# Kernel tuning notes

Hardware: AMD Instinct MI355X
Metric: run time of the kernel (lower is better)

Reference implementation:

```python
import jax, jax.numpy as jnp
import numpy as np

B, IN_DIM, OUT_DIM = 16384, 1024, 512
N_CAPS, CAP_DIM = 8, 16


def squash(x, axis=-1):
    # scale = |x|^2 / (1 + |x|^2) ; out = scale * x / sqrt(|x|^2 + 1e-8)
    sq = jnp.sum(x * x, axis=axis, keepdims=True)
    return (sq / (1.0 + sq)) * x / jnp.sqrt(sq + 1e-8)


def setup_inputs() -> dict:
    key = jax.random.key(0)
    k1, k2, k3, k4 = jax.random.split(key, 4)
    x = jax.random.normal(k1, (B, IN_DIM), dtype=jnp.float32)
    # Linear(in_dim, n_caps*cap_dim) params (kaiming-ish scale)
    Wp = jax.random.normal(k2, (IN_DIM, N_CAPS * CAP_DIM), dtype=jnp.float32) / np.sqrt(IN_DIM)
    bp = jax.random.normal(k3, (N_CAPS * CAP_DIM,), dtype=jnp.float32) * 0.01
    # routing transform W: [n_caps, cap_dim, out_dim], init std 0.02 as in torch code
    W = jax.random.normal(k4, (N_CAPS, CAP_DIM, OUT_DIM), dtype=jnp.float32) * 0.02
    return {"x": x, "Wp": Wp, "bp": bp, "W": W, "n_routing": 3}


def reference(x, Wp, bp, W, n_routing):
    batch = x.shape[0]
    primary = x @ Wp + bp                                   # [B, n*d]
    primary = primary.reshape(batch, N_CAPS, CAP_DIM)       # [B, n, d]
    primary = squash(primary, axis=-1)
    u_hat = jnp.einsum('bnd,ndo->bno', primary, W)          # [B, n, o]
    b = jnp.zeros((batch, N_CAPS, 1), dtype=x.dtype)
    v = None
    for i in range(n_routing):
        c = jax.nn.softmax(b, axis=1)                       # [B, n, 1]
        s = jnp.sum(c * u_hat, axis=1)                      # [B, o]
        v = squash(s, axis=-1)                              # [B, o]
        if i < n_routing - 1:
            agreement = jnp.einsum('bno,bo->bn', u_hat, v)  # [B, n]
            b = b + agreement[..., None]
    return v
```

## Files before the change

kernel.cpp:

```cpp
#include <hip/hip_runtime.h>
#include <hip/hip_bf16.h>
#include <math.h>

typedef __attribute__((ext_vector_type(8))) short bf16x8;
typedef __attribute__((ext_vector_type(8))) unsigned short u16x8;
typedef __attribute__((ext_vector_type(4))) float f32x4;
typedef __attribute__((ext_vector_type(16))) float f32x16;

__device__ __forceinline__ unsigned short f2bf(float f) {
  unsigned u = __float_as_uint(f);
  return (unsigned short)((u + 0x7FFFu + ((u >> 16) & 1u)) >> 16);
}
__device__ __forceinline__ float bf2f(unsigned short h) {
  return __uint_as_float(((unsigned)h) << 16);
}
__device__ __forceinline__ void cvt8pk_a(const float* f, u16x8& h, u16x8& l) {
  unsigned* hp = (unsigned*)&h;
  unsigned* lp = (unsigned*)&l;
#pragma unroll
  for (int i = 0; i < 4; ++i) {
    __hip_bfloat162 hb = __float22bfloat162_rn(make_float2(f[2*i], f[2*i+1]));
    unsigned hv = *(unsigned*)&hb;
    hp[i] = hv;
    float r0 = f[2*i]     - __uint_as_float(hv << 16);
    float r1 = f[2*i + 1] - __uint_as_float(hv & 0xFFFF0000u);
    __hip_bfloat162 lb = __float22bfloat162_rn(make_float2(r0, r1));
    lp[i] = *(unsigned*)&lb;
  }
}
__device__ __forceinline__ void cvt8pk(const float4& a, const float4& b,
                                       u16x8& h, u16x8& l) {
  float f[8] = {a.x, a.y, a.z, a.w, b.x, b.y, b.z, b.w};
  cvt8pk_a(f, h, l);
}
__device__ __forceinline__ void cvt8b(const float4& a, const float4& b,
                                      bf16x8& h, bf16x8& l) {
  u16x8 hh, ll;
  cvt8pk(a, b, hh, ll);
  h = *(bf16x8*)&hh;
  l = *(bf16x8*)&ll;
}

#define GLD16(g, l) __builtin_amdgcn_global_load_lds( \
    (const __attribute__((address_space(1))) void*)(g), \
    (__attribute__((address_space(3))) void*)(l), 16, 0, 0)

#define MFMA32(a, b, c) __builtin_amdgcn_mfma_f32_32x32x16_bf16(a, b, c, 0, 0, 0)

__global__ __launch_bounds__(256) void caps_prep_all(
    const float* __restrict__ Wp, const float* __restrict__ W,
    unsigned short* __restrict__ th1, unsigned short* __restrict__ tl1,
    unsigned short* __restrict__ th2, unsigned short* __restrict__ tl2,
    unsigned short* __restrict__ th3, unsigned short* __restrict__ tl3)
{
  __shared__ float tile[64][128];
  const int t = threadIdx.x, b = blockIdx.x;
  if (b < 16) {
    const float* src = Wp + (size_t)b * 64 * 128;
#pragma unroll
    for (int i = 0; i < 8; ++i) {
      int j = t + i * 256;
      int kk = j >> 5, q = j & 31;
      *(float4*)&tile[kk][q * 4] = *(const float4*)(src + kk * 128 + q * 4);
    }
    __syncthreads();
    const int col = t >> 1, kg0 = (t & 1) * 4;
    unsigned short hi[32], lo[32];
#pragma unroll
    for (int kk = 0; kk < 32; ++kk) {
      float v = tile[kg0 * 8 + kk][col];
      unsigned short h = f2bf(v);
      hi[kk] = h;
      lo[kk] = f2bf(v - bf2f(h));
    }
#pragma unroll
    for (int i = 0; i < 4; ++i) {
      size_t off = (size_t)b * 8192 + (size_t)(kg0 + i) * 1024 + (size_t)col * 8;
      u16x8 vh, vl;
#pragma unroll
      for (int e = 0; e < 8; ++e) { vh[e] = hi[i * 8 + e]; vl[e] = lo[i * 8 + e]; }
      *(u16x8*)(th1 + off) = vh;
      *(u16x8*)(tl1 + off) = vl;
    }
  } else if (b < 32) {
    int tt = (b - 16) * 256 + t;
#pragma unroll
    for (int h = 0; h < 2; ++h) {
      int c = tt + h * 4096;
      int kt = c >> 12, rem = c & 4095;
      int kg = rem >> 9, col = rem & 511;
      int kbase = kt * 64 + kg * 8;
      u16x8 vh, vl;
#pragma unroll
      for (int e = 0; e < 8; ++e) {
        float v = W[(size_t)(kbase + e) * 512 + col];
        unsigned short hh = f2bf(v);
        vh[e] = hh;
        vl[e] = f2bf(v - bf2f(hh));
      }
      size_t off = ((size_t)(kt * 8 + kg) * 512 + col) * 8;
      *(u16x8*)(th2 + off) = vh;
      *(u16x8*)(tl2 + off) = vl;
    }
  } else {
    int bb = b - 32;
    int a = (bb >> 3) * 16 + (t >> 4);
    int c = (bb & 7) * 16 + (t & 15);
    const float* wa = W + (size_t)a * 512;
    const float* wb = W + (size_t)c * 512;
    float acc = 0.f;
#pragma unroll 4
    for (int o = 0; o < 512; o += 4) {
      float4 xx = *(const float4*)(wa + o);
      float4 yy = *(const float4*)(wb + o);
      acc += xx.x * yy.x + xx.y * yy.y + xx.z * yy.z + xx.w * yy.w;
    }
    unsigned short h = f2bf(acc);
    unsigned short l = f2bf(acc - bf2f(h));
    size_t off = ((size_t)(a >> 3) * 128 + c) * 8 + (a & 7);
    th3[off] = h;
    tl3[off] = l;
  }
}

#define K1BUF 20480

__global__ __launch_bounds__(256) void caps_primary(
    const float* __restrict__ x, const unsigned short* __restrict__ bth,
    const unsigned short* __restrict__ btl, const float* __restrict__ bp,
    float* __restrict__ p_out)
{
  __shared__ unsigned short lds[2 * K1BUF];
  const int tid  = threadIdx.x;
  const int lane = tid & 63;
  const int wn   = tid >> 6;
  const int lc   = lane & 31;
  const int hi   = lane >> 5;
  const int row0 = blockIdx.x * 32;

  const int rowA = tid & 31;
  const int kgA  = tid >> 5;
  const float* xrow = x + (size_t)(row0 + rowA) * 1024 + kgA * 8;

  f32x16 acc;
#pragma unroll
  for (int j = 0; j < 16; ++j) acc[j] = 0.f;

  float4 a0, a1;

#define A_LOAD(kt) do { const float* xp_ = xrow + (kt) * 64; \
    a0 = *(const float4*)(xp_); a1 = *(const float4*)(xp_ + 4); } while (0)

#define B_ISSUE(kt, bufi) do { \
    unsigned short* Bh_ = lds + (bufi) * K1BUF + 4096; \
    unsigned short* Bl_ = lds + (bufi) * K1BUF + 12288; \
    const unsigned short* gh_ = bth + ((size_t)(kt) * 1024 + tid) * 8; \
    const unsigned short* gl_ = btl + ((size_t)(kt) * 1024 + tid) * 8; \
    _Pragma("unroll") for (int c_ = 0; c_ < 4; ++c_) { \
      GLD16(gh_ + c_ * 2048, Bh_ + (c_ * 256 + tid) * 8); \
      GLD16(gl_ + c_ * 2048, Bl_ + (c_ * 256 + tid) * 8); \
    } } while (0)

#define A_WRITE(bufi) do { u16x8 h_, l_; cvt8pk(a0, a1, h_, l_); \
    unsigned short* A_ = lds + (bufi) * K1BUF; \
    *(u16x8*)(A_ + (kgA * 32 + rowA) * 8) = h_; \
    *(u16x8*)(A_ + 2048 + (kgA * 32 + rowA) * 8) = l_; } while (0)

#define COMPUTE(bufi) do { \
    const unsigned short* F = lds + (bufi) * K1BUF; \
    _Pragma("unroll") \
    for (int kk = 0; kk < 4; ++kk) { \
      const int ks = kk * 2 + hi; \
      bf16x8 ah  = *(const bf16x8*)(F + (ks * 32 + lc) * 8); \
      bf16x8 al  = *(const bf16x8*)(F + 2048 + (ks * 32 + lc) * 8); \
      bf16x8 bh  = *(const bf16x8*)(F + 4096  + (ks * 128 + wn * 32 + lc) * 8); \
      bf16x8 blo = *(const bf16x8*)(F + 12288 + (ks * 128 + wn * 32 + lc) * 8); \
      acc = MFMA32(ah, bh,  acc); \
      acc = MFMA32(ah, blo, acc); \
      acc = MFMA32(al, bh,  acc); \
    } } while (0)

  A_LOAD(0);
  B_ISSUE(0, 0);
  A_WRITE(0);
  __syncthreads();

#pragma unroll 2
  for (int kt = 0; kt < 16; ++kt) {
    const int cur = kt & 1;
    if (kt < 15) {
      A_LOAD(kt + 1);
      B_ISSUE(kt + 1, cur ^ 1);
    }
    COMPUTE(cur);
    if (kt < 15) A_WRITE(cur ^ 1);
    __syncthreads();
  }
#undef A_LOAD
#undef B_ISSUE
#undef A_WRITE
#undef COMPUTE

  const int col = wn * 32 + lc;
  const float bpv = bp[col];
#pragma unroll
  for (int r = 0; r < 16; ++r) {
    const int row = (r & 3) + 8 * (r >> 2) + 4 * hi;
    float val = acc[r] + bpv;
    float sq = val * val;
    sq += __shfl_xor(sq, 1); sq += __shfl_xor(sq, 2);
    sq += __shfl_xor(sq, 4); sq += __shfl_xor(sq, 8);
    float sc = (sq / (1.f + sq)) / sqrtf(sq + 1e-8f);
    p_out[(size_t)(row0 + row) * 128 + col] = val * sc;
  }
}

__global__ __launch_bounds__(512) void caps_route_g(
    const float* __restrict__ p_in, const unsigned short* __restrict__ mh,
    const unsigned short* __restrict__ ml, float* __restrict__ cs_out)
{
  __shared__ float pT[128 * 65];
  __shared__ unsigned short Msh[32768];
  __shared__ float t_lds[64 * 9];
  __shared__ float c_lds[64 * 9];
  const int tid  = threadIdx.x;
  const int lane = tid & 63;
  const int w    = tid >> 6;
  const int wm   = w >> 2;
  const int wn   = w & 3;
  const int lc   = lane & 31;
  const int hi   = lane >> 5;
  const int row0 = blockIdx.x * 64;

#pragma unroll
  for (int i = 0; i < 4; ++i) {
    int idx = tid + i * 512;
    *(u16x8*)&Msh[idx * 8] = *(const u16x8*)(mh + (size_t)idx * 8);
    *(u16x8*)&Msh[16384 + idx * 8] = *(const u16x8*)(ml + (size_t)idx * 8);
  }
#pragma unroll
  for (int i = 0; i < 4; ++i) {
    int j = tid + i * 512;
    int r = j >> 5, c4 = j & 31;
    f32x4 v = *(const f32x4*)(p_in + (size_t)(row0 + r) * 128 + c4 * 4);
    pT[(c4 * 4 + 0) * 65 + r] = v[0];
    pT[(c4 * 4 + 1) * 65 + r] = v[1];
    pT[(c4 * 4 + 2) * 65 + r] = v[2];
    pT[(c4 * 4 + 3) * 65 + r] = v[3];
  }
  if (w == 0) {
#pragma unroll
    for (int n = 0; n < 8; ++n) c_lds[lane * 9 + n] = 0.125f;
  }
  __syncthreads();

  const int arow = wm * 32 + lc;
  const int col  = wn * 32 + lc;
  const int cap  = wn * 2 + (lc >> 4);
  float bb[8] = {0.f, 0.f, 0.f, 0.f, 0.f, 0.f, 0.f, 0.f};

#pragma unroll 1
  for (int it = 0; it < 3; ++it) {
    f32x16 acc;
#pragma unroll
    for (int j = 0; j < 16; ++j) acc[j] = 0.f;

#pragma unroll
    for (int kk = 0; kk < 8; ++kk) {
      const float cv = c_lds[arow * 9 + kk];
      float q[8];
#pragma unroll
      for (int e = 0; e < 8; ++e)
        q[e] = pT[(kk * 16 + hi * 8 + e) * 65 + arow] * cv;
      u16x8 hq, lq;
      cvt8pk_a(q, hq, lq);
      const int fi = ((kk * 2 + hi) * 128 + col) * 8;
      bf16x8 mbh = *(const bf16x8*)&Msh[fi];
      bf16x8 mbl = *(const bf16x8*)&Msh[16384 + fi];
      acc = MFMA32(*(bf16x8*)&hq, mbh, acc);
      acc = MFMA32(*(bf16x8*)&hq, mbl, acc);
      acc = MFMA32(*(bf16x8*)&lq, mbh, acc);
    }

    float tp[16];
#pragma unroll
    for (int r = 0; r < 16; ++r) {
      const int row = wm * 32 + (r & 3) + 8 * (r >> 2) + 4 * hi;
      float prod = pT[col * 65 + row] * acc[r];
      prod += __shfl_xor(prod, 1);
      prod += __shfl_xor(prod, 2);
      prod += __shfl_xor(prod, 4);
      prod += __shfl_xor(prod, 8);
      tp[r] = prod;
    }
    __syncthreads();
    if ((lc & 15) == 0) {
#pragma unroll
      for (int r = 0; r < 16; ++r) {
        const int row = wm * 32 + (r & 3) + 8 * (r >> 2) + 4 * hi;
        t_lds[row * 9 + cap] = tp[r];
      }
    }
    __syncthreads();

    if (w == 0) {
      float c[8], t[8];
#pragma unroll
      for (int n = 0; n < 8; ++n) {
        c[n] = c_lds[lane * 9 + n];
        t[n] = t_lds[lane * 9 + n];
      }
      float ss = 0.f;
#pragma unroll
      for (int n = 0; n < 8; ++n) ss = fmaf(c[n], t[n], ss);
      float scale = (ss / (1.f + ss)) / sqrtf(ss + 1e-8f);
      if (it < 2) {
#pragma unroll
        for (int n = 0; n < 8; ++n) bb[n] += scale * t[n];
        float mx = bb[0];
#pragma unroll
        for (int n = 1; n < 8; ++n) mx = fmaxf(mx, bb[n]);
        float e[8], Z = 0.f;
#pragma unroll
        for (int n = 0; n < 8; ++n) { e[n] = expf(bb[n] - mx); Z += e[n]; }
        float inv = 1.f / Z;
#pragma unroll
        for (int n = 0; n < 8; ++n) c_lds[lane * 9 + n] = e[n] * inv;
      } else {
        f32x4 c0 = {scale * c[0], scale * c[1], scale * c[2], scale * c[3]};
        f32x4 c1 = {scale * c[4], scale * c[5], scale * c[6], scale * c[7]};
        *(f32x4*)(cs_out + (size_t)(row0 + lane) * 8)     = c0;
        *(f32x4*)(cs_out + (size_t)(row0 + lane) * 8 + 4) = c1;
      }
    }
    __syncthreads();
  }
}

__global__ __launch_bounds__(512) void caps_vout(
    const float* __restrict__ p, const unsigned short* __restrict__ bth,
    const unsigned short* __restrict__ btl, const float* __restrict__ cs,
    float* __restrict__ out)
{
  __shared__ unsigned short Bsh[32768];
  const int tid  = threadIdx.x;
  const int lane = tid & 63;
  const int w    = tid >> 6;
  const int wm   = w >> 2;
  const int wn   = w & 3;
  const int lc   = lane & 31;
  const int hi   = lane >> 5;
  const int row0 = blockIdx.x * 64;
  const int col0 = blockIdx.y * 128;

#pragma unroll
  for (int i = 0; i < 4; ++i) {
    int idx = tid + i * 512;
    int kt = idx >> 10, kg = (idx >> 7) & 7, col = idx & 127;
    size_t g = ((size_t)(kt * 8 + kg) * 512 + col0 + col) * 8;
    *(u16x8*)&Bsh[idx * 8] = *(const u16x8*)(bth + g);
    *(u16x8*)&Bsh[16384 + idx * 8] = *(const u16x8*)(btl + g);
  }

  const int rA = row0 + wm * 32 + lc;
  const float* qp = p + (size_t)rA * 128;
  float cs8[8];
  *(f32x4*)&cs8[0] = *(const f32x4*)(cs + (size_t)rA * 8);
  *(f32x4*)&cs8[4] = *(const f32x4*)(cs + (size_t)rA * 8 + 4);
  __syncthreads();

  f32x16 acc;
#pragma unroll
  for (int j = 0; j < 16; ++j) acc[j] = 0.f;

#pragma unroll
  for (int kt = 0; kt < 2; ++kt) {
#pragma unroll
    for (int kk = 0; kk < 4; ++kk) {
      const float* qk = qp + kt * 64 + kk * 16 + hi * 8;
      float4 a0 = *(const float4*)(qk);
      float4 a1 = *(const float4*)(qk + 4);
      const float cv = cs8[kt * 4 + kk];
      a0.x *= cv; a0.y *= cv; a0.z *= cv; a0.w *= cv;
      a1.x *= cv; a1.y *= cv; a1.z *= cv; a1.w *= cv;
      bf16x8 ah, al;
      cvt8b(a0, a1, ah, al);
      const int ks = kk * 2 + hi;
      const int fi = ((kt * 8 + ks) * 128 + wn * 32 + lc) * 8;
      bf16x8 bh  = *(const bf16x8*)&Bsh[fi];
      bf16x8 blo = *(const bf16x8*)&Bsh[16384 + fi];
      acc = MFMA32(ah, bh,  acc);
      acc = MFMA32(ah, blo, acc);
      acc = MFMA32(al, bh,  acc);
    }
  }

#pragma unroll
  for (int r = 0; r < 16; ++r) {
    const int row = (r & 3) + 8 * (r >> 2) + 4 * hi;
    out[(size_t)(row0 + wm * 32 + row) * 512 + col0 + wn * 32 + lc] = acc[r];
  }
}

extern "C" void kernel_launch(void* const* d_in, const int* in_sizes, int n_in,
                              void* d_out, int out_size, void* d_ws, size_t ws_size,
                              hipStream_t stream) {
  (void)in_sizes; (void)n_in; (void)out_size; (void)ws_size;
  const float* x  = (const float*)d_in[0];
  const float* Wp = (const float*)d_in[1];
  const float* bp = (const float*)d_in[2];
  const float* W  = (const float*)d_in[3];
  char* ws = (char*)d_ws;
  float* p_ws = (float*)ws;
  unsigned short* th1 = (unsigned short*)(ws + 8388608);
  unsigned short* tl1 = (unsigned short*)(ws + 8650752);
  unsigned short* th2 = (unsigned short*)(ws + 8912896);
  unsigned short* tl2 = (unsigned short*)(ws + 9043968);
  unsigned short* th3 = (unsigned short*)(ws + 9175040);
  unsigned short* tl3 = (unsigned short*)(ws + 9207808);
  float* cs_ws = (float*)(ws + 9240576);
  float* outp = (float*)d_out;

  caps_prep_all<<<96, 256, 0, stream>>>(Wp, W, th1, tl1, th2, tl2, th3, tl3);
  caps_primary<<<512, 256, 0, stream>>>(x, th1, tl1, bp, p_ws);
  caps_route_g<<<256, 512, 0, stream>>>(p_ws, th3, tl3, cs_ws);
  caps_vout<<<dim3(256, 4), 512, 0, stream>>>(p_ws, th2, tl2, cs_ws, outp);
}
```

Measured before the change: 84.26 us.

## Double primary GEMM row tile to 64 and stage B through registers

The primary projection kernel now handles 64 rows per block with 512 threads arranged as 2x4 waves, halving the grid to 256 blocks so each loaded weight tile is reused across twice as many rows. The async global-to-LDS loads for the B operand are replaced by ordinary register loads that are written to LDS alongside the converted A tile. This cuts redundant weight traffic, at the cost of fewer blocks (256 on a large-CU GPU), more LDS per block and extra register pressure from holding B in registers.

```diff
diff --git a/kernel.cpp b/kernel.cpp
--- a/kernel.cpp
+++ b/kernel.cpp
@@ -40,10 +40,6 @@
   h = *(bf16x8*)&hh;
   l = *(bf16x8*)&ll;
 }
-
-#define GLD16(g, l) __builtin_amdgcn_global_load_lds( \
-    (const __attribute__((address_space(1))) void*)(g), \
-    (__attribute__((address_space(3))) void*)(l), 16, 0, 0)
 
 #define MFMA32(a, b, c) __builtin_amdgcn_mfma_f32_32x32x16_bf16(a, b, c, 0, 0, 0)
 
@@ -123,9 +119,9 @@
   }
 }
 
-#define K1BUF 20480
-
-__global__ __launch_bounds__(256) void caps_primary(
+#define K1BUF 24576
+
+__global__ __launch_bounds__(512) void caps_primary(
     const float* __restrict__ x, const unsigned short* __restrict__ bth,
     const unsigned short* __restrict__ btl, const float* __restrict__ bp,
     float* __restrict__ p_out)
@@ -133,13 +129,15 @@
   __shared__ unsigned short lds[2 * K1BUF];
   const int tid  = threadIdx.x;
   const int lane = tid & 63;
-  const int wn   = tid >> 6;
+  const int w    = tid >> 6;
+  const int wm   = w >> 2;
+  const int wn   = w & 3;
   const int lc   = lane & 31;
   const int hi   = lane >> 5;
-  const int row0 = blockIdx.x * 32;
-
-  const int rowA = tid & 31;
-  const int kgA  = tid >> 5;
+  const int row0 = blockIdx.x * 64;
+
+  const int rowA = tid & 63;
+  const int kgA  = tid >> 6;
   const float* xrow = x + (size_t)(row0 + rowA) * 1024 + kgA * 8;
 
   f32x16 acc;
@@ -147,42 +145,45 @@
   for (int j = 0; j < 16; ++j) acc[j] = 0.f;
 
   float4 a0, a1;
+  u16x8 b0, b1, b2, b3;
 
 #define A_LOAD(kt) do { const float* xp_ = xrow + (kt) * 64; \
     a0 = *(const float4*)(xp_); a1 = *(const float4*)(xp_ + 4); } while (0)
 
-#define B_ISSUE(kt, bufi) do { \
-    unsigned short* Bh_ = lds + (bufi) * K1BUF + 4096; \
-    unsigned short* Bl_ = lds + (bufi) * K1BUF + 12288; \
-    const unsigned short* gh_ = bth + ((size_t)(kt) * 1024 + tid) * 8; \
-    const unsigned short* gl_ = btl + ((size_t)(kt) * 1024 + tid) * 8; \
-    _Pragma("unroll") for (int c_ = 0; c_ < 4; ++c_) { \
-      GLD16(gh_ + c_ * 2048, Bh_ + (c_ * 256 + tid) * 8); \
-      GLD16(gl_ + c_ * 2048, Bl_ + (c_ * 256 + tid) * 8); \
-    } } while (0)
-
-#define A_WRITE(bufi) do { u16x8 h_, l_; cvt8pk(a0, a1, h_, l_); \
-    unsigned short* A_ = lds + (bufi) * K1BUF; \
-    *(u16x8*)(A_ + (kgA * 32 + rowA) * 8) = h_; \
-    *(u16x8*)(A_ + 2048 + (kgA * 32 + rowA) * 8) = l_; } while (0)
+#define B_LOAD(kt) do { \
+    const unsigned short* gh_ = bth + ((size_t)(kt) * 1024) * 8; \
+    const unsigned short* gl_ = btl + ((size_t)(kt) * 1024) * 8; \
+    b0 = *(const u16x8*)(gh_ + (size_t)tid * 8); \
+    b1 = *(const u16x8*)(gh_ + (size_t)(512 + tid) * 8); \
+    b2 = *(const u16x8*)(gl_ + (size_t)tid * 8); \
+    b3 = *(const u16x8*)(gl_ + (size_t)(512 + tid) * 8); } while (0)
+
+#define AB_WRITE(bufi) do { u16x8 h_, l_; cvt8pk(a0, a1, h_, l_); \
+    unsigned short* B_ = lds + (bufi) * K1BUF; \
+    *(u16x8*)(B_ + (kgA * 64 + rowA) * 8) = h_; \
+    *(u16x8*)(B_ + 4096 + (kgA * 64 + rowA) * 8) = l_; \
+    *(u16x8*)(B_ + 8192  + tid * 8) = b0; \
+    *(u16x8*)(B_ + 8192  + (512 + tid) * 8) = b1; \
+    *(u16x8*)(B_ + 16384 + tid * 8) = b2; \
+    *(u16x8*)(B_ + 16384 + (512 + tid) * 8) = b3; } while (0)
 
 #define COMPUTE(bufi) do { \
     const unsigned short* F = lds + (bufi) * K1BUF; \
     _Pragma("unroll") \
     for (int kk = 0; kk < 4; ++kk) { \
       const int ks = kk * 2 + hi; \
-      bf16x8 ah  = *(const bf16x8*)(F + (ks * 32 + lc) * 8); \
-      bf16x8 al  = *(const bf16x8*)(F + 2048 + (ks * 32 + lc) * 8); \
-      bf16x8 bh  = *(const bf16x8*)(F + 4096  + (ks * 128 + wn * 32 + lc) * 8); \
-      bf16x8 blo = *(const bf16x8*)(F + 12288 + (ks * 128 + wn * 32 + lc) * 8); \
+      bf16x8 ah  = *(const bf16x8*)(F + (ks * 64 + wm * 32 + lc) * 8); \
+      bf16x8 al  = *(const bf16x8*)(F + 4096 + (ks * 64 + wm * 32 + lc) * 8); \
+      bf16x8 bh  = *(const bf16x8*)(F + 8192  + (ks * 128 + wn * 32 + lc) * 8); \
+      bf16x8 blo = *(const bf16x8*)(F + 16384 + (ks * 128 + wn * 32 + lc) * 8); \
       acc = MFMA32(ah, bh,  acc); \
       acc = MFMA32(ah, blo, acc); \
       acc = MFMA32(al, bh,  acc); \
     } } while (0)
 
   A_LOAD(0);
-  B_ISSUE(0, 0);
-  A_WRITE(0);
+  B_LOAD(0);
+  AB_WRITE(0);
   __syncthreads();
 
 #pragma unroll 2
@@ -190,22 +191,22 @@
     const int cur = kt & 1;
     if (kt < 15) {
       A_LOAD(kt + 1);
-      B_ISSUE(kt + 1, cur ^ 1);
+      B_LOAD(kt + 1);
     }
     COMPUTE(cur);
-    if (kt < 15) A_WRITE(cur ^ 1);
+    if (kt < 15) AB_WRITE(cur ^ 1);
     __syncthreads();
   }
 #undef A_LOAD
-#undef B_ISSUE
-#undef A_WRITE
+#undef B_LOAD
+#undef AB_WRITE
 #undef COMPUTE
 
   const int col = wn * 32 + lc;
   const float bpv = bp[col];
 #pragma unroll
   for (int r = 0; r < 16; ++r) {
-    const int row = (r & 3) + 8 * (r >> 2) + 4 * hi;
+    const int row = wm * 32 + (r & 3) + 8 * (r >> 2) + 4 * hi;
     float val = acc[r] + bpv;
     float sq = val * val;
     sq += __shfl_xor(sq, 1); sq += __shfl_xor(sq, 2);
@@ -422,7 +423,7 @@
   float* outp = (float*)d_out;
 
   caps_prep_all<<<96, 256, 0, stream>>>(Wp, W, th1, tl1, th2, tl2, th3, tl3);
-  caps_primary<<<512, 256, 0, stream>>>(x, th1, tl1, bp, p_ws);
+  caps_primary<<<256, 512, 0, stream>>>(x, th1, tl1, bp, p_ws);
   caps_route_g<<<256, 512, 0, stream>>>(p_ws, th3, tl3, cs_ws);
   caps_vout<<<dim3(256, 4), 512, 0, stream>>>(p_ws, th2, tl2, cs_ws, outp);
 }
```

Result: no change. 85.83 us, median of 2 (+1.9%).

## Retile primary projection to 16-row blocks with 16x16x32 MFMA, single-buffered

Applied to the files above, without the earlier changes.

The primary projection GEMM now uses 16-row tiles with 16x16x32 bf16 MFMAs. Each wave covers two 16-column fragments, and the grid doubles to 1024 blocks. The double-buffered prefetch pipeline is replaced by a simple load, sync, compute, sync loop, and only half the threads convert x rows. The aim is more resident blocks per CU, through less LDS per block and more blocks, to hide load latency. In exchange, the Wp tiles are reloaded twice as often overall, and load/compute overlap within a block is lost.

```diff
diff --git a/kernel.cpp b/kernel.cpp
--- a/kernel.cpp
+++ b/kernel.cpp
@@ -45,6 +45,7 @@
     (const __attribute__((address_space(1))) void*)(g), \
     (__attribute__((address_space(3))) void*)(l), 16, 0, 0)
 
+#define MFMA16(a, b, c) __builtin_amdgcn_mfma_f32_16x16x32_bf16(a, b, c, 0, 0, 0)
 #define MFMA32(a, b, c) __builtin_amdgcn_mfma_f32_32x32x16_bf16(a, b, c, 0, 0, 0)
 
 __global__ __launch_bounds__(256) void caps_prep_all(
@@ -123,95 +124,80 @@
   }
 }
 
-#define K1BUF 20480
-
 __global__ __launch_bounds__(256) void caps_primary(
     const float* __restrict__ x, const unsigned short* __restrict__ bth,
     const unsigned short* __restrict__ btl, const float* __restrict__ bp,
     float* __restrict__ p_out)
 {
-  __shared__ unsigned short lds[2 * K1BUF];
+  __shared__ unsigned short lds[18432];
   const int tid  = threadIdx.x;
   const int lane = tid & 63;
-  const int wn   = tid >> 6;
-  const int lc   = lane & 31;
-  const int hi   = lane >> 5;
-  const int row0 = blockIdx.x * 32;
-
-  const int rowA = tid & 31;
-  const int kgA  = tid >> 5;
+  const int w    = tid >> 6;
+  const int cb   = lane & 15;
+  const int kgl  = lane >> 4;
+  const int row0 = blockIdx.x * 16;
+
+  const int rowA = (tid & 127) >> 3;
+  const int kgA  = tid & 7;
   const float* xrow = x + (size_t)(row0 + rowA) * 1024 + kgA * 8;
 
-  f32x16 acc;
-#pragma unroll
-  for (int j = 0; j < 16; ++j) acc[j] = 0.f;
-
-  float4 a0, a1;
-
-#define A_LOAD(kt) do { const float* xp_ = xrow + (kt) * 64; \
-    a0 = *(const float4*)(xp_); a1 = *(const float4*)(xp_ + 4); } while (0)
-
-#define B_ISSUE(kt, bufi) do { \
-    unsigned short* Bh_ = lds + (bufi) * K1BUF + 4096; \
-    unsigned short* Bl_ = lds + (bufi) * K1BUF + 12288; \
-    const unsigned short* gh_ = bth + ((size_t)(kt) * 1024 + tid) * 8; \
-    const unsigned short* gl_ = btl + ((size_t)(kt) * 1024 + tid) * 8; \
-    _Pragma("unroll") for (int c_ = 0; c_ < 4; ++c_) { \
-      GLD16(gh_ + c_ * 2048, Bh_ + (c_ * 256 + tid) * 8); \
-      GLD16(gl_ + c_ * 2048, Bl_ + (c_ * 256 + tid) * 8); \
-    } } while (0)
-
-#define A_WRITE(bufi) do { u16x8 h_, l_; cvt8pk(a0, a1, h_, l_); \
-    unsigned short* A_ = lds + (bufi) * K1BUF; \
-    *(u16x8*)(A_ + (kgA * 32 + rowA) * 8) = h_; \
-    *(u16x8*)(A_ + 2048 + (kgA * 32 + rowA) * 8) = l_; } while (0)
-
-#define COMPUTE(bufi) do { \
-    const unsigned short* F = lds + (bufi) * K1BUF; \
-    _Pragma("unroll") \
-    for (int kk = 0; kk < 4; ++kk) { \
-      const int ks = kk * 2 + hi; \
-      bf16x8 ah  = *(const bf16x8*)(F + (ks * 32 + lc) * 8); \
-      bf16x8 al  = *(const bf16x8*)(F + 2048 + (ks * 32 + lc) * 8); \
-      bf16x8 bh  = *(const bf16x8*)(F + 4096  + (ks * 128 + wn * 32 + lc) * 8); \
-      bf16x8 blo = *(const bf16x8*)(F + 12288 + (ks * 128 + wn * 32 + lc) * 8); \
-      acc = MFMA32(ah, bh,  acc); \
-      acc = MFMA32(ah, blo, acc); \
-      acc = MFMA32(al, bh,  acc); \
-    } } while (0)
-
-  A_LOAD(0);
-  B_ISSUE(0, 0);
-  A_WRITE(0);
-  __syncthreads();
-
-#pragma unroll 2
+  f32x4 acc[2];
+  acc[0] = (f32x4){0.f, 0.f, 0.f, 0.f};
+  acc[1] = (f32x4){0.f, 0.f, 0.f, 0.f};
+
   for (int kt = 0; kt < 16; ++kt) {
-    const int cur = kt & 1;
-    if (kt < 15) {
-      A_LOAD(kt + 1);
-      B_ISSUE(kt + 1, cur ^ 1);
-    }
-    COMPUTE(cur);
-    if (kt < 15) A_WRITE(cur ^ 1);
-    __syncthreads();
-  }
-#undef A_LOAD
-#undef B_ISSUE
-#undef A_WRITE
-#undef COMPUTE
-
-  const int col = wn * 32 + lc;
-  const float bpv = bp[col];
-#pragma unroll
-  for (int r = 0; r < 16; ++r) {
-    const int row = (r & 3) + 8 * (r >> 2) + 4 * hi;
-    float val = acc[r] + bpv;
-    float sq = val * val;
-    sq += __shfl_xor(sq, 1); sq += __shfl_xor(sq, 2);
-    sq += __shfl_xor(sq, 4); sq += __shfl_xor(sq, 8);
-    float sc = (sq / (1.f + sq)) / sqrtf(sq + 1e-8f);
-    p_out[(size_t)(row0 + row) * 128 + col] = val * sc;
+    {
+      const unsigned short* gh = bth + (size_t)kt * 8192 + (size_t)tid * 8;
+      const unsigned short* gl = btl + (size_t)kt * 8192 + (size_t)tid * 8;
+#pragma unroll
+      for (int c = 0; c < 4; ++c) {
+        GLD16(gh + c * 2048, lds + 2048  + (c * 256 + tid) * 8);
+        GLD16(gl + c * 2048, lds + 10240 + (c * 256 + tid) * 8);
+      }
+    }
+    if (tid < 128) {
+      const float* xp = xrow + kt * 64;
+      float4 a0 = *(const float4*)(xp);
+      float4 a1 = *(const float4*)(xp + 4);
+      u16x8 h_, l_;
+      cvt8pk(a0, a1, h_, l_);
+      *(u16x8*)(lds + (kgA * 16 + rowA) * 8) = h_;
+      *(u16x8*)(lds + 1024 + (kgA * 16 + rowA) * 8) = l_;
+    }
+    __syncthreads();
+
+#pragma unroll
+    for (int s = 0; s < 2; ++s) {
+      const int ks = s * 4 + kgl;
+      bf16x8 ah = *(const bf16x8*)(lds + (ks * 16 + cb) * 8);
+      bf16x8 al = *(const bf16x8*)(lds + 1024 + (ks * 16 + cb) * 8);
+#pragma unroll
+      for (int nf = 0; nf < 2; ++nf) {
+        const int col = w * 32 + nf * 16 + cb;
+        bf16x8 bh  = *(const bf16x8*)(lds + 2048  + (ks * 128 + col) * 8);
+        bf16x8 blo = *(const bf16x8*)(lds + 10240 + (ks * 128 + col) * 8);
+        acc[nf] = MFMA16(ah, bh,  acc[nf]);
+        acc[nf] = MFMA16(ah, blo, acc[nf]);
+        acc[nf] = MFMA16(al, bh,  acc[nf]);
+      }
+    }
+    __syncthreads();
+  }
+
+  const int l4 = lane >> 4;
+#pragma unroll
+  for (int nf = 0; nf < 2; ++nf) {
+    const int col = w * 32 + nf * 16 + cb;
+    const float bpv = bp[col];
+#pragma unroll
+    for (int r = 0; r < 4; ++r) {
+      float val = acc[nf][r] + bpv;
+      float sq = val * val;
+      sq += __shfl_xor(sq, 1); sq += __shfl_xor(sq, 2);
+      sq += __shfl_xor(sq, 4); sq += __shfl_xor(sq, 8);
+      float sc = (sq / (1.f + sq)) / sqrtf(sq + 1e-8f);
+      p_out[(size_t)(row0 + l4 * 4 + r) * 128 + col] = val * sc;
+    }
   }
 }
 
@@ -422,7 +408,7 @@
   float* outp = (float*)d_out;
 
   caps_prep_all<<<96, 256, 0, stream>>>(Wp, W, th1, tl1, th2, tl2, th3, tl3);
-  caps_primary<<<512, 256, 0, stream>>>(x, th1, tl1, bp, p_ws);
+  caps_primary<<<1024, 256, 0, stream>>>(x, th1, tl1, bp, p_ws);
   caps_route_g<<<256, 512, 0, stream>>>(p_ws, th3, tl3, cs_ws);
   caps_vout<<<dim3(256, 4), 512, 0, stream>>>(p_ws, th2, tl2, cs_ws, outp);
 }
```

Result: slower. 93.77 us (+11.3%).

## Drop LDS staging in primary GEMM, load operands directly into registers

Applied to the files above, without the earlier changes.

The primary projection kernel no longer stages x and the split-bf16 weights through double-buffered LDS with barriers. Each wave now loads its A fragments (fp32 x rows) and B fragments straight from global memory into registers, converts A to hi/lo bf16 in registers, and software-pipelines two register buffers using sched_barrier fences. This removes the LDS traffic and the per-iteration __syncthreads. In exchange, each of the 4 waves re-reads the same x rows, so A global traffic rises fourfold, and register pressure goes up.

```diff
diff --git a/kernel.cpp b/kernel.cpp
--- a/kernel.cpp
+++ b/kernel.cpp
@@ -41,11 +41,8 @@
   l = *(bf16x8*)&ll;
 }
 
-#define GLD16(g, l) __builtin_amdgcn_global_load_lds( \
-    (const __attribute__((address_space(1))) void*)(g), \
-    (__attribute__((address_space(3))) void*)(l), 16, 0, 0)
-
 #define MFMA32(a, b, c) __builtin_amdgcn_mfma_f32_32x32x16_bf16(a, b, c, 0, 0, 0)
+#define SB0() __builtin_amdgcn_sched_barrier(0)
 
 __global__ __launch_bounds__(256) void caps_prep_all(
     const float* __restrict__ Wp, const float* __restrict__ W,
@@ -123,14 +120,11 @@
   }
 }
 
-#define K1BUF 20480
-
 __global__ __launch_bounds__(256) void caps_primary(
     const float* __restrict__ x, const unsigned short* __restrict__ bth,
     const unsigned short* __restrict__ btl, const float* __restrict__ bp,
     float* __restrict__ p_out)
 {
-  __shared__ unsigned short lds[2 * K1BUF];
   const int tid  = threadIdx.x;
   const int lane = tid & 63;
   const int wn   = tid >> 6;
@@ -138,71 +132,74 @@
   const int hi   = lane >> 5;
   const int row0 = blockIdx.x * 32;
 
-  const int rowA = tid & 31;
-  const int kgA  = tid >> 5;
-  const float* xrow = x + (size_t)(row0 + rowA) * 1024 + kgA * 8;
+  const int colB = wn * 32 + lc;
+  const float* xrowA = x + (size_t)(row0 + lc) * 1024 + hi * 8;
+  const bf16x8* Bh = (const bf16x8*)bth;
+  const bf16x8* Bl = (const bf16x8*)btl;
 
   f32x16 acc;
 #pragma unroll
   for (int j = 0; j < 16; ++j) acc[j] = 0.f;
 
-  float4 a0, a1;
-
-#define A_LOAD(kt) do { const float* xp_ = xrow + (kt) * 64; \
-    a0 = *(const float4*)(xp_); a1 = *(const float4*)(xp_ + 4); } while (0)
-
-#define B_ISSUE(kt, bufi) do { \
-    unsigned short* Bh_ = lds + (bufi) * K1BUF + 4096; \
-    unsigned short* Bl_ = lds + (bufi) * K1BUF + 12288; \
-    const unsigned short* gh_ = bth + ((size_t)(kt) * 1024 + tid) * 8; \
-    const unsigned short* gl_ = btl + ((size_t)(kt) * 1024 + tid) * 8; \
-    _Pragma("unroll") for (int c_ = 0; c_ < 4; ++c_) { \
-      GLD16(gh_ + c_ * 2048, Bh_ + (c_ * 256 + tid) * 8); \
-      GLD16(gl_ + c_ * 2048, Bl_ + (c_ * 256 + tid) * 8); \
-    } } while (0)
-
-#define A_WRITE(bufi) do { u16x8 h_, l_; cvt8pk(a0, a1, h_, l_); \
-    unsigned short* A_ = lds + (bufi) * K1BUF; \
-    *(u16x8*)(A_ + (kgA * 32 + rowA) * 8) = h_; \
-    *(u16x8*)(A_ + 2048 + (kgA * 32 + rowA) * 8) = l_; } while (0)
-
-#define COMPUTE(bufi) do { \
-    const unsigned short* F = lds + (bufi) * K1BUF; \
+  float4 XA0[8], XA1[8];
+  bf16x8 BH0[4], BL0[4], BH1[4], BL1[4];
+
+#define A_LOAD(kt, XA) do { const float* xp_ = xrowA + (kt) * 64; \
+    XA[0] = *(const float4*)(xp_);      XA[1] = *(const float4*)(xp_ + 4); \
+    XA[2] = *(const float4*)(xp_ + 16); XA[3] = *(const float4*)(xp_ + 20); \
+    XA[4] = *(const float4*)(xp_ + 32); XA[5] = *(const float4*)(xp_ + 36); \
+    XA[6] = *(const float4*)(xp_ + 48); XA[7] = *(const float4*)(xp_ + 52); } while (0)
+
+#define B_LOAD(kt, BH, BL) do { \
+    const size_t kb_ = (size_t)(kt) * 1024 + colB; \
+    BH[0] = Bh[kb_ + (0 * 2 + hi) * 128]; \
+    BH[1] = Bh[kb_ + (1 * 2 + hi) * 128]; \
+    BH[2] = Bh[kb_ + (2 * 2 + hi) * 128]; \
+    BH[3] = Bh[kb_ + (3 * 2 + hi) * 128]; \
+    BL[0] = Bl[kb_ + (0 * 2 + hi) * 128]; \
+    BL[1] = Bl[kb_ + (1 * 2 + hi) * 128]; \
+    BL[2] = Bl[kb_ + (2 * 2 + hi) * 128]; \
+    BL[3] = Bl[kb_ + (3 * 2 + hi) * 128]; } while (0)
+
+#define COMPUTE(XA, BH, BL) do { \
     _Pragma("unroll") \
     for (int kk = 0; kk < 4; ++kk) { \
-      const int ks = kk * 2 + hi; \
-      bf16x8 ah  = *(const bf16x8*)(F + (ks * 32 + lc) * 8); \
-      bf16x8 al  = *(const bf16x8*)(F + 2048 + (ks * 32 + lc) * 8); \
-      bf16x8 bh  = *(const bf16x8*)(F + 4096  + (ks * 128 + wn * 32 + lc) * 8); \
-      bf16x8 blo = *(const bf16x8*)(F + 12288 + (ks * 128 + wn * 32 + lc) * 8); \
-      acc = MFMA32(ah, bh,  acc); \
-      acc = MFMA32(ah, blo, acc); \
-      acc = MFMA32(al, bh,  acc); \
+      u16x8 hq, lq; \
+      cvt8pk(XA[2 * kk], XA[2 * kk + 1], hq, lq); \
+      acc = MFMA32(*(bf16x8*)&hq, BH[kk], acc); \
+      acc = MFMA32(*(bf16x8*)&hq, BL[kk], acc); \
+      acc = MFMA32(*(bf16x8*)&lq, BH[kk], acc); \
     } } while (0)
 
-  A_LOAD(0);
-  B_ISSUE(0, 0);
-  A_WRITE(0);
-  __syncthreads();
-
-#pragma unroll 2
-  for (int kt = 0; kt < 16; ++kt) {
-    const int cur = kt & 1;
-    if (kt < 15) {
-      A_LOAD(kt + 1);
-      B_ISSUE(kt + 1, cur ^ 1);
-    }
-    COMPUTE(cur);
-    if (kt < 15) A_WRITE(cur ^ 1);
-    __syncthreads();
-  }
+  A_LOAD(0, XA0);
+  B_LOAD(0, BH0, BL0);
+  SB0();
+
+#pragma unroll 1
+  for (int kt = 0; kt < 14; kt += 2) {
+    A_LOAD(kt + 1, XA1);
+    B_LOAD(kt + 1, BH1, BL1);
+    SB0();
+    COMPUTE(XA0, BH0, BL0);
+    SB0();
+    A_LOAD(kt + 2, XA0);
+    B_LOAD(kt + 2, BH0, BL0);
+    SB0();
+    COMPUTE(XA1, BH1, BL1);
+    SB0();
+  }
+  A_LOAD(15, XA1);
+  B_LOAD(15, BH1, BL1);
+  SB0();
+  COMPUTE(XA0, BH0, BL0);
+  SB0();
+  COMPUTE(XA1, BH1, BL1);
+
 #undef A_LOAD
-#undef B_ISSUE
-#undef A_WRITE
+#undef B_LOAD
 #undef COMPUTE
 
-  const int col = wn * 32 + lc;
-  const float bpv = bp[col];
+  const float bpv = bp[colB];
 #pragma unroll
   for (int r = 0; r < 16; ++r) {
     const int row = (r & 3) + 8 * (r >> 2) + 4 * hi;
@@ -211,7 +208,7 @@
     sq += __shfl_xor(sq, 1); sq += __shfl_xor(sq, 2);
     sq += __shfl_xor(sq, 4); sq += __shfl_xor(sq, 8);
     float sc = (sq / (1.f + sq)) / sqrtf(sq + 1e-8f);
-    p_out[(size_t)(row0 + row) * 128 + col] = val * sc;
+    p_out[(size_t)(row0 + row) * 128 + colB] = val * sc;
   }
 }
 
```

Measured after the change: 101.6 us. 20.5% more time.
